# Kernel optimization log

Hardware: AMD Instinct MI355X
Metric: run time of the kernel (lower is better)

Reference implementation:

```python
import jax, jax.numpy as jnp
import numpy as np

GRID = 8        # proto_grid_size
THRESH = 0.95   # prototype selection threshold
EPS = 1e-4      # safe_norm eps
TEMP = 20.0     # cosine-similarity temperature
NEG_INF = -1e9

def safe_norm(x, axis):
    n = jnp.maximum(jnp.linalg.norm(x, axis=axis, keepdims=True), EPS)
    return x / n

def avg_pool(x, k):
    # [B, C, H, W] -> [B, C, H//k, W//k], non-overlapping average pooling
    B, C, H, W = x.shape
    return x.reshape(B, C, H // k, k, W // k, k).mean(axis=(3, 5))

def setup_inputs() -> dict:
    key = jax.random.key(0)
    k1, k2 = jax.random.split(key)
    qry = jax.random.normal(k1, (16, 512, 64, 64), dtype=jnp.float32)
    sup_x = jax.random.normal(k2, (16, 512, 64, 64), dtype=jnp.float32)
    sup_y = jnp.ones((16, 1, 64, 64), dtype=jnp.float32)
    return {"qry": qry, "sup_x": sup_x, "sup_y": sup_y}

def reference(qry, sup_x, sup_y):
    # mode='gridconv', thresh=0.95 (module defaults)
    B, C, H, W = sup_x.shape
    k = H // GRID  # avg-pool kernel size

    # normalize query features over channels (safe_norm with dim=1)
    qry_n = safe_norm(qry, axis=1)

    # grid prototypes: avg-pool support features, flatten to [B*G*G, C]
    n_sup = avg_pool(sup_x, k)                                   # [B, C, G, G]
    n_sup = n_sup.reshape(B, C, -1).transpose(0, 2, 1).reshape(-1, C)

    # pooled mask grid and thresholding
    sup_y_g = avg_pool(sup_y, k)                                 # [B, 1, G, G]
    proto_grid = jnp.where(sup_y_g < THRESH, 0.0, sup_y_g)
    valid = sup_y_g.reshape(-1) > THRESH                          # [P] bool

    # normalized prototypes (per-row; masking handles unselected cells)
    protos = safe_norm(n_sup, axis=1)                             # [P, C]

    # 1x1-conv similarity == channel contraction, scaled by temperature
    dists = jnp.einsum('bchw,pc->bphw', qry_n, protos) * TEMP     # [B, P, Hq, Wq]
    logits = jnp.where(valid[None, :, None, None], dists, NEG_INF)

    # softmax-weighted sum over prototypes (invalid protos get exactly 0 weight)
    p = jax.nn.softmax(logits, axis=1)
    vals = jnp.where(valid[None, :, None, None], dists, 0.0)
    pred = jnp.sum(p * vals, axis=1, keepdims=True)               # [B, 1, Hq, Wq]

    debug_assign = jnp.argmax(logits, axis=1).astype(jnp.float32)
    return pred, debug_assign, proto_grid
```

## Files before the change

### kernel.cpp

```cpp
#include <hip/hip_runtime.h>
#include <math.h>

#define B_      16
#define C_      512
#define HW_     4096
#define P_      1024
#define EPSN    1e-4f
#define TEMP_   20.0f
#define THRESH_ 0.95f
#define NEGINF_ -1e9f
#define TIE_THR 1e-3f

#define PRED_OFF   0
#define ASSIGN_OFF 65536
#define GRID_OFF   131072

typedef short short8 __attribute__((ext_vector_type(8)));
typedef float f32x16 __attribute__((ext_vector_type(16)));

__device__ inline unsigned short f2bf(float f) {
    unsigned u = __float_as_uint(f);
    unsigned r = u + 0x7fffu + ((u >> 16) & 1u);
    return (unsigned short)(r >> 16);
}
__device__ inline float bf2f(unsigned short h) {
    return __uint_as_float((unsigned)h << 16);
}

__global__ void pool_y_kernel(const float* __restrict__ sup_y,
                              float* __restrict__ out_grid,
                              float* __restrict__ validf) {
    int p = blockIdx.x * blockDim.x + threadIdx.x;
    if (p >= P_) return;
    int b = p >> 6, cell = p & 63, gy = cell >> 3, gx = cell & 7;
    const float* base = sup_y + b * HW_ + gy * 8 * 64 + gx * 8;
    float s = 0.f;
    #pragma unroll
    for (int r = 0; r < 8; ++r)
        #pragma unroll
        for (int c = 0; c < 8; ++c) s += base[r * 64 + c];
    float avg = s * (1.0f / 64.0f);
    out_grid[p] = (avg < THRESH_) ? 0.0f : avg;
    validf[p]   = (avg > THRESH_) ? 1.0f : 0.0f;
}

__global__ __launch_bounds__(256) void pool_x_kernel(const float* __restrict__ sup_x,
                                                     float* __restrict__ pooledT) {
    int blk = blockIdx.x * 4 + (threadIdx.x >> 6);
    int b = blk >> 9, c = blk & 511;
    int lane = threadIdx.x & 63;
    const float* base = sup_x + (size_t)(b * C_ + c) * HW_;
    float acc[8];
    #pragma unroll
    for (int g = 0; g < 8; ++g) acc[g] = 0.f;
    #pragma unroll
    for (int h = 0; h < 64; ++h) {
        float v = base[h * 64 + lane];
        acc[h >> 3] += v;
    }
    #pragma unroll
    for (int g = 0; g < 8; ++g) {
        acc[g] += __shfl_xor(acc[g], 1);
        acc[g] += __shfl_xor(acc[g], 2);
        acc[g] += __shfl_xor(acc[g], 4);
    }
    if ((lane & 7) == 0) {
        int gx = lane >> 3;
        #pragma unroll
        for (int gy = 0; gy < 8; ++gy) {
            int p = b * 64 + gy * 8 + gx;
            pooledT[c * P_ + p] = acc[gy] * (1.0f / 64.0f);
        }
    }
}

__global__ __launch_bounds__(512) void pack_b_kernel(const float* __restrict__ pooledT,
                                                     const float* __restrict__ validf,
                                                     short* __restrict__ Bph,
                                                     short* __restrict__ Bpl,
                                                     float* __restrict__ rnv) {
    __shared__ double ssred[8][64];
    int nl = threadIdx.x & 63;
    int w  = threadIdx.x >> 6;
    int n  = blockIdx.x * 64 + nl;
    double ss = 0.0;
    for (int c8i = 0; c8i < 8; ++c8i) {
        int c8 = w * 8 + c8i;
        unsigned short vh[8], vl[8];
        #pragma unroll
        for (int j = 0; j < 8; ++j) {
            float p = pooledT[(c8 * 8 + j) * P_ + n];
            ss += (double)p * (double)p;
            unsigned short h = f2bf(p);
            vh[j] = h;
            vl[j] = f2bf(p - bf2f(h));
        }
        uint4 uh, ul;
        uh.x = (unsigned)vh[0] | ((unsigned)vh[1] << 16);
        uh.y = (unsigned)vh[2] | ((unsigned)vh[3] << 16);
        uh.z = (unsigned)vh[4] | ((unsigned)vh[5] << 16);
        uh.w = (unsigned)vh[6] | ((unsigned)vh[7] << 16);
        ul.x = (unsigned)vl[0] | ((unsigned)vl[1] << 16);
        ul.y = (unsigned)vl[2] | ((unsigned)vl[3] << 16);
        ul.z = (unsigned)vl[4] | ((unsigned)vl[5] << 16);
        ul.w = (unsigned)vl[6] | ((unsigned)vl[7] << 16);
        int sk = c8 >> 1, kh = c8 & 1;
        *(uint4*)&Bph[sk * 16384 + n * 16 + kh * 8] = uh;
        *(uint4*)&Bpl[sk * 16384 + n * 16 + kh * 8] = ul;
    }
    ssred[w][nl] = ss;
    __syncthreads();
    if (threadIdx.x < 64) {
        double s = 0.0;
        #pragma unroll
        for (int q = 0; q < 8; ++q) s += ssred[q][threadIdx.x];
        int nn = blockIdx.x * 64 + threadIdx.x;
        float rn = 1.0f / fmaxf((float)sqrt(s), EPSN);
        rnv[nn] = (validf[nn] > 0.5f) ? rn : 0.0f;
    }
}

__global__ __launch_bounds__(512, 2) void gemm_fused_kernel(
        const float* __restrict__ qry,
        const short* __restrict__ Bph,
        const short* __restrict__ Bpl,
        const float* __restrict__ pooledT,
        const float* __restrict__ rnv,
        float* __restrict__ out) {
    __shared__ short Ah2[32 * 1024];
    __shared__ short Al2[32 * 1024];

    float* ss_tab  = (float*)Ah2;
    float* rq_s    = (float*)Ah2 + 512;
    float* stbuf   = (float*)Ah2 + 576;
    int*   rowinfo = (int*)((float*)Ah2 + 576 + 64 * 8 * 6);

    int m0 = blockIdx.x * 64;
    int b = m0 >> 12;
    int hw0 = m0 & 4095;
    int tid = threadIdx.x;
    int w = tid >> 6;
    int lane = tid & 63;
    int hl = lane & 31, half = lane >> 5;
    int nb = w * 128;

    const float* qb = qry + (size_t)b * (C_ * HW_) + hw0;
    const short* bh_base = Bph + ((nb + hl) * 16 + half * 8);
    const short* bl_base = Bpl + ((nb + hl) * 16 + half * 8);

    f32x16 zero16 = {0.f,0.f,0.f,0.f,0.f,0.f,0.f,0.f,0.f,0.f,0.f,0.f,0.f,0.f,0.f,0.f};
    f32x16 acc[2][4];
    #pragma unroll
    for (int mt = 0; mt < 2; ++mt)
        #pragma unroll
        for (int nt = 0; nt < 4; ++nt) acc[mt][nt] = zero16;

    short8 bhc[4], blc[4];
    #pragma unroll
    for (int nt = 0; nt < 4; ++nt) {
        bhc[nt] = *(const short8*)(bh_base + nt * 512);
        blc[nt] = *(const short8*)(bl_base + nt * 512);
    }

    float ss = 0.f;
    #pragma unroll
    for (int g = 0; g < 8; ++g) {
        int idx16 = g * 8 + w;
        const float* qp = qb + (size_t)(idx16 * 8) * HW_ + lane;
        float q[8];
        #pragma unroll
        for (int j = 0; j < 8; ++j) q[j] = qp[(size_t)j * HW_];
        uint4 UH, UL;
        unsigned uh[4], ul[4];
        #pragma unroll
        for (int jj = 0; jj < 4; ++jj) {
            float a0 = q[2 * jj], a1 = q[2 * jj + 1];
            unsigned short h0 = f2bf(a0), h1 = f2bf(a1);
            float r0 = a0 - bf2f(h0), r1 = a1 - bf2f(h1);
            unsigned short l0 = f2bf(r0), l1 = f2bf(r1);
            uh[jj] = (unsigned)h0 | ((unsigned)h1 << 16);
            ul[jj] = (unsigned)l0 | ((unsigned)l1 << 16);
            ss += a0 * a0 + a1 * a1;
        }
        UH.x = uh[0]; UH.y = uh[1]; UH.z = uh[2]; UH.w = uh[3];
        UL.x = ul[0]; UL.y = ul[1]; UL.z = ul[2]; UL.w = ul[3];
        int off = (idx16 * 64 + lane) * 8;
        *(uint4*)&Ah2[off] = UH;
        *(uint4*)&Al2[off] = UL;
    }
    __syncthreads();

    int abase = half * 512 + hl * 8;
    short8 ahc[2], alc[2];
    #pragma unroll
    for (int mt = 0; mt < 2; ++mt) {
        ahc[mt] = *(const short8*)&Ah2[abase + mt * 256];
        alc[mt] = *(const short8*)&Al2[abase + mt * 256];
    }

    for (int sk = 0; sk < 32; ++sk) {
        int nsk = sk + 1;
        short8 bhn[4], bln[4], ahn[2], aln[2];
        if (nsk < 32) {
            const short* bh_p = bh_base + nsk * 16384;
            const short* bl_p = bl_base + nsk * 16384;
            #pragma unroll
            for (int nt = 0; nt < 4; ++nt) {
                bhn[nt] = *(const short8*)(bh_p + nt * 512);
                bln[nt] = *(const short8*)(bl_p + nt * 512);
            }
            int ao = nsk * 1024 + abase;
            #pragma unroll
            for (int mt = 0; mt < 2; ++mt) {
                ahn[mt] = *(const short8*)&Ah2[ao + mt * 256];
                aln[mt] = *(const short8*)&Al2[ao + mt * 256];
            }
        }
        #pragma unroll
        for (int nt = 0; nt < 4; ++nt) {
            #pragma unroll
            for (int mt = 0; mt < 2; ++mt) {
                acc[mt][nt] = __builtin_amdgcn_mfma_f32_32x32x16_bf16(ahc[mt], bhc[nt], acc[mt][nt], 0, 0, 0);
                acc[mt][nt] = __builtin_amdgcn_mfma_f32_32x32x16_bf16(alc[mt], bhc[nt], acc[mt][nt], 0, 0, 0);
                acc[mt][nt] = __builtin_amdgcn_mfma_f32_32x32x16_bf16(ahc[mt], blc[nt], acc[mt][nt], 0, 0, 0);
            }
        }
        if (nsk < 32) {
            #pragma unroll
            for (int nt = 0; nt < 4; ++nt) { bhc[nt] = bhn[nt]; blc[nt] = bln[nt]; }
            #pragma unroll
            for (int mt = 0; mt < 2; ++mt) { ahc[mt] = ahn[mt]; alc[mt] = aln[mt]; }
        }
    }
    __syncthreads();

    ss_tab[w * 64 + lane] = ss;
    __syncthreads();
    if (tid < 64) {
        float s = 0.f;
        #pragma unroll
        for (int q = 0; q < 8; ++q) s += ss_tab[q * 64 + tid];
        rq_s[tid] = 1.0f / fmaxf(sqrtf(s), EPSN);
    }
    __syncthreads();

    float rn4[4];
    #pragma unroll
    for (int nt = 0; nt < 4; ++nt) rn4[nt] = rnv[nb + nt * 32 + hl];

    #pragma unroll
    for (int mt = 0; mt < 2; ++mt) {
        #pragma unroll
        for (int r = 0; r < 16; ++r) {
            int mrow = mt * 32 + (r & 3) + 8 * (r >> 2) + 4 * half;
            float scale = rq_s[mrow] * TEMP_;
            float d4[4], lg4[4];
            float v1 = -3e38f, v2 = -3e38f;
            int n1 = P_, n2 = P_;
            #pragma unroll
            for (int nt = 0; nt < 4; ++nt) {
                float dd = acc[mt][nt][r] * rn4[nt] * scale;
                float lg = (rn4[nt] > 0.f) ? dd : NEGINF_;
                d4[nt] = dd; lg4[nt] = lg;
                int n = nb + nt * 32 + hl;
                if (lg > v1 || (lg == v1 && n < n1)) {
                    v2 = v1; n2 = n1; v1 = lg; n1 = n;
                } else if (lg > v2 || (lg == v2 && n < n2)) {
                    v2 = lg; n2 = n;
                }
            }
            #pragma unroll
            for (int off = 1; off < 32; off <<= 1) {
                float ov1 = __shfl_xor(v1, off), ov2 = __shfl_xor(v2, off);
                int   on1 = __shfl_xor(n1, off), on2 = __shfl_xor(n2, off);
                if (ov1 > v1 || (ov1 == v1 && on1 < n1)) {
                    if (v1 > ov2 || (v1 == ov2 && n1 < on2)) { v2 = v1; n2 = n1; }
                    else                                     { v2 = ov2; n2 = on2; }
                    v1 = ov1; n1 = on1;
                } else {
                    if (ov1 > v2 || (ov1 == v2 && on1 < n2)) { v2 = ov1; n2 = on1; }
                }
            }
            float se = 0.f, sv = 0.f;
            #pragma unroll
            for (int nt = 0; nt < 4; ++nt) {
                float e = __expf(lg4[nt] - v1);
                se += e;
                sv += e * d4[nt];
            }
            #pragma unroll
            for (int off = 1; off < 32; off <<= 1) {
                se += __shfl_xor(se, off);
                sv += __shfl_xor(sv, off);
            }
            if (hl == 0) {
                float* s6 = stbuf + (mrow * 8 + w) * 6;
                s6[0] = v1; s6[1] = v2;
                s6[2] = __int_as_float(n1); s6[3] = __int_as_float(n2);
                s6[4] = se; s6[5] = sv;
            }
        }
    }
    __syncthreads();

    {
        int row = w * 8 + (lane >> 3), s = lane & 7;
        const float* s6 = stbuf + (row * 8 + s) * 6;
        float v1 = s6[0], v2 = s6[1];
        int n1 = __float_as_int(s6[2]), n2 = __float_as_int(s6[3]);
        float se = s6[4], sv = s6[5];
        #pragma unroll
        for (int off = 1; off < 8; off <<= 1) {
            float ov1 = __shfl_xor(v1, off), ov2 = __shfl_xor(v2, off);
            int   on1 = __shfl_xor(n1, off), on2 = __shfl_xor(n2, off);
            float ose = __shfl_xor(se, off), osv = __shfl_xor(sv, off);
            float myv1 = v1;
            float mv1, mv2; int mn1, mn2;
            if (ov1 > v1 || (ov1 == v1 && on1 < n1)) {
                mv1 = ov1; mn1 = on1;
                if (v1 > ov2 || (v1 == ov2 && n1 < on2)) { mv2 = v1; mn2 = n1; }
                else                                     { mv2 = ov2; mn2 = on2; }
            } else {
                mv1 = v1; mn1 = n1;
                if (ov1 > v2 || (ov1 == v2 && on1 < n2)) { mv2 = ov1; mn2 = on1; }
                else                                     { mv2 = v2; mn2 = n2; }
            }
            float fa = __expf(myv1 - mv1), fb = __expf(ov1 - mv1);
            se = se * fa + ose * fb;
            sv = sv * fa + osv * fb;
            v1 = mv1; n1 = mn1; v2 = mv2; n2 = mn2;
        }
        if (s == 0) {
            int gm = m0 + row;
            out[PRED_OFF + gm] = sv / se;
            bool flagged = (n2 < P_) && ((v1 - v2) < TIE_THR);
            if (!flagged) out[ASSIGN_OFF + gm] = (float)n1;
            rowinfo[row] = flagged ? (n1 | (n2 << 16)) : -1;
        }
    }
    __syncthreads();

    if (w == 0) {
        for (int row = 0; row < 64; ++row) {
            int info = rowinfo[row];
            if (info < 0) continue;
            int n1 = info & 0xffff, n2 = info >> 16;
            const float* qcol = qb + row;
            double d1 = 0.0, d2 = 0.0, s1 = 0.0, s2 = 0.0;
            for (int cc = lane; cc < C_; cc += 64) {
                double qv = (double)qcol[(size_t)cc * HW_];
                double p1 = (double)pooledT[cc * P_ + n1];
                double p2 = (double)pooledT[cc * P_ + n2];
                d1 += qv * p1; d2 += qv * p2;
                s1 += p1 * p1; s2 += p2 * p2;
            }
            #pragma unroll
            for (int off = 1; off < 64; off <<= 1) {
                d1 += __shfl_xor(d1, off); d2 += __shfl_xor(d2, off);
                s1 += __shfl_xor(s1, off); s2 += __shfl_xor(s2, off);
            }
            double f1 = d1 / fmax(sqrt(s1), (double)EPSN);
            double f2 = d2 / fmax(sqrt(s2), (double)EPSN);
            int best = (f2 > f1 || (f2 == f1 && n2 < n1)) ? n2 : n1;
            if (lane == 0) out[ASSIGN_OFF + m0 + row] = (float)best;
        }
    }
}

extern "C" void kernel_launch(void* const* d_in, const int* in_sizes, int n_in,
                              void* d_out, int out_size, void* d_ws, size_t ws_size,
                              hipStream_t stream) {
    const float* qry   = (const float*)d_in[0];
    const float* sup_x = (const float*)d_in[1];
    const float* sup_y = (const float*)d_in[2];
    float* out = (float*)d_out;
    float* ws  = (float*)d_ws;

    float* pooledT = ws;
    float* rnv     = pooledT + C_ * P_;
    float* validf  = rnv + P_;
    short* Bph     = (short*)(validf + P_);
    short* Bpl     = Bph + 32 * 1024 * 16;

    pool_y_kernel<<<4, 256, 0, stream>>>(sup_y, out + GRID_OFF, validf);
    pool_x_kernel<<<B_ * C_ / 4, 256, 0, stream>>>(sup_x, pooledT);
    pack_b_kernel<<<16, 512, 0, stream>>>(pooledT, validf, Bph, Bpl, rnv);
    gemm_fused_kernel<<<B_ * HW_ / 64, 512, 0, stream>>>(qry, Bph, Bpl, pooledT, rnv, out);
}
```

Measured before the change: 642.3 us.

## Vectorize pooling and query loads, double-buffer MFMA operands with setprio

```diff
diff --git a/kernel.cpp b/kernel.cpp
--- a/kernel.cpp
+++ b/kernel.cpp
@@ -49,28 +49,28 @@
     int blk = blockIdx.x * 4 + (threadIdx.x >> 6);
     int b = blk >> 9, c = blk & 511;
     int lane = threadIdx.x & 63;
+    int cq = lane & 15, rq = lane >> 4;
     const float* base = sup_x + (size_t)(b * C_ + c) * HW_;
     float acc[8];
     #pragma unroll
     for (int g = 0; g < 8; ++g) acc[g] = 0.f;
     #pragma unroll
-    for (int h = 0; h < 64; ++h) {
-        float v = base[h * 64 + lane];
-        acc[h >> 3] += v;
+    for (int i = 0; i < 16; ++i) {
+        int row = 4 * i + rq;
+        float4 v = *(const float4*)(base + row * 64 + cq * 4);
+        acc[i >> 1] += (v.x + v.y) + (v.z + v.w);
     }
     #pragma unroll
     for (int g = 0; g < 8; ++g) {
         acc[g] += __shfl_xor(acc[g], 1);
-        acc[g] += __shfl_xor(acc[g], 2);
-        acc[g] += __shfl_xor(acc[g], 4);
-    }
-    if ((lane & 7) == 0) {
-        int gx = lane >> 3;
-        #pragma unroll
-        for (int gy = 0; gy < 8; ++gy) {
-            int p = b * 64 + gy * 8 + gx;
-            pooledT[c * P_ + p] = acc[gy] * (1.0f / 64.0f);
-        }
+        acc[g] += __shfl_xor(acc[g], 16);
+        acc[g] += __shfl_xor(acc[g], 32);
+    }
+    if (rq == 0 && (cq & 1) == 0) {
+        int gx = cq >> 1;
+        #pragma unroll
+        for (int gy = 0; gy < 8; ++gy)
+            pooledT[c * P_ + b * 64 + gy * 8 + gx] = acc[gy] * (1.0f / 64.0f);
     }
 }
 
@@ -129,11 +129,11 @@
         float* __restrict__ out) {
     __shared__ short Ah2[32 * 1024];
     __shared__ short Al2[32 * 1024];
-
-    float* ss_tab  = (float*)Ah2;
-    float* rq_s    = (float*)Ah2 + 512;
-    float* stbuf   = (float*)Ah2 + 576;
-    int*   rowinfo = (int*)((float*)Ah2 + 576 + 64 * 8 * 6);
+    __shared__ float ss_part[512 * 4];
+    __shared__ float rqs_lds[64];
+
+    float* stbuf   = (float*)Ah2;
+    int*   rowinfo = (int*)((float*)Ah2 + 64 * 8 * 6);
 
     int m0 = blockIdx.x * 64;
     int b = m0 >> 12;
@@ -155,92 +155,122 @@
         #pragma unroll
         for (int nt = 0; nt < 4; ++nt) acc[mt][nt] = zero16;
 
-    short8 bhc[4], blc[4];
+    short8 bh0[4], bl0[4], bh1[4], bl1[4];
+    short8 ah0[2], al0[2], ah1[2], al1[2];
     #pragma unroll
     for (int nt = 0; nt < 4; ++nt) {
-        bhc[nt] = *(const short8*)(bh_base + nt * 512);
-        blc[nt] = *(const short8*)(bl_base + nt * 512);
-    }
-
-    float ss = 0.f;
-    #pragma unroll
-    for (int g = 0; g < 8; ++g) {
-        int idx16 = g * 8 + w;
-        const float* qp = qb + (size_t)(idx16 * 8) * HW_ + lane;
-        float q[8];
-        #pragma unroll
-        for (int j = 0; j < 8; ++j) q[j] = qp[(size_t)j * HW_];
-        uint4 UH, UL;
-        unsigned uh[4], ul[4];
-        #pragma unroll
-        for (int jj = 0; jj < 4; ++jj) {
-            float a0 = q[2 * jj], a1 = q[2 * jj + 1];
-            unsigned short h0 = f2bf(a0), h1 = f2bf(a1);
-            float r0 = a0 - bf2f(h0), r1 = a1 - bf2f(h1);
-            unsigned short l0 = f2bf(r0), l1 = f2bf(r1);
-            uh[jj] = (unsigned)h0 | ((unsigned)h1 << 16);
-            ul[jj] = (unsigned)l0 | ((unsigned)l1 << 16);
-            ss += a0 * a0 + a1 * a1;
-        }
-        UH.x = uh[0]; UH.y = uh[1]; UH.z = uh[2]; UH.w = uh[3];
-        UL.x = ul[0]; UL.y = ul[1]; UL.z = ul[2]; UL.w = ul[3];
-        int off = (idx16 * 64 + lane) * 8;
-        *(uint4*)&Ah2[off] = UH;
-        *(uint4*)&Al2[off] = UL;
+        bh0[nt] = *(const short8*)(bh_base + nt * 512);
+        bl0[nt] = *(const short8*)(bl_base + nt * 512);
+    }
+
+    {
+        int pg = tid & 15;
+        int c8a = tid >> 4;
+        float ss4[4] = {0.f, 0.f, 0.f, 0.f};
+        #pragma unroll
+        for (int un = 0; un < 2; ++un) {
+            int c8 = c8a + un * 32;
+            const float* src = qb + (size_t)(c8 * 8) * HW_ + pg * 4;
+            float4 q[8];
+            #pragma unroll
+            for (int j = 0; j < 8; ++j)
+                q[j] = *(const float4*)(src + (size_t)j * HW_);
+            #pragma unroll
+            for (int pp = 0; pp < 4; ++pp) {
+                unsigned uh[4], ul[4];
+                #pragma unroll
+                for (int jj = 0; jj < 4; ++jj) {
+                    float a0 = ((const float*)&q[2 * jj])[pp];
+                    float a1 = ((const float*)&q[2 * jj + 1])[pp];
+                    unsigned short h0 = f2bf(a0), h1 = f2bf(a1);
+                    float r0 = a0 - bf2f(h0), r1 = a1 - bf2f(h1);
+                    unsigned short l0 = f2bf(r0), l1 = f2bf(r1);
+                    uh[jj] = (unsigned)h0 | ((unsigned)h1 << 16);
+                    ul[jj] = (unsigned)l0 | ((unsigned)l1 << 16);
+                    ss4[pp] += a0 * a0 + a1 * a1;
+                }
+                uint4 UH, UL;
+                UH.x = uh[0]; UH.y = uh[1]; UH.z = uh[2]; UH.w = uh[3];
+                UL.x = ul[0]; UL.y = ul[1]; UL.z = ul[2]; UL.w = ul[3];
+                int off = (c8 * 64 + pg * 4 + pp) * 8;
+                *(uint4*)&Ah2[off] = UH;
+                *(uint4*)&Al2[off] = UL;
+            }
+        }
+        *(float4*)&ss_part[tid * 4] = *(float4*)ss4;
     }
     __syncthreads();
 
+    if (tid < 64) {
+        int pg = tid >> 2, pp = tid & 3;
+        float s = 0.f;
+        #pragma unroll
+        for (int k = 0; k < 32; ++k) s += ss_part[(pg + 16 * k) * 4 + pp];
+        rqs_lds[tid] = 1.0f / fmaxf(sqrtf(s), EPSN);
+    }
+
     int abase = half * 512 + hl * 8;
-    short8 ahc[2], alc[2];
     #pragma unroll
     for (int mt = 0; mt < 2; ++mt) {
-        ahc[mt] = *(const short8*)&Ah2[abase + mt * 256];
-        alc[mt] = *(const short8*)&Al2[abase + mt * 256];
-    }
-
-    for (int sk = 0; sk < 32; ++sk) {
-        int nsk = sk + 1;
-        short8 bhn[4], bln[4], ahn[2], aln[2];
-        if (nsk < 32) {
-            const short* bh_p = bh_base + nsk * 16384;
-            const short* bl_p = bl_base + nsk * 16384;
+        ah0[mt] = *(const short8*)&Ah2[abase + mt * 256];
+        al0[mt] = *(const short8*)&Al2[abase + mt * 256];
+    }
+
+    for (int skp = 0; skp < 16; ++skp) {
+        int sk1 = skp * 2 + 1;
+        int sk2 = (skp < 15) ? (skp * 2 + 2) : 31;
+        {
+            const short* bh_p = bh_base + sk1 * 16384;
+            const short* bl_p = bl_base + sk1 * 16384;
             #pragma unroll
             for (int nt = 0; nt < 4; ++nt) {
-                bhn[nt] = *(const short8*)(bh_p + nt * 512);
-                bln[nt] = *(const short8*)(bl_p + nt * 512);
-            }
-            int ao = nsk * 1024 + abase;
+                bh1[nt] = *(const short8*)(bh_p + nt * 512);
+                bl1[nt] = *(const short8*)(bl_p + nt * 512);
+            }
+            int ao = sk1 * 1024 + abase;
             #pragma unroll
             for (int mt = 0; mt < 2; ++mt) {
-                ahn[mt] = *(const short8*)&Ah2[ao + mt * 256];
-                aln[mt] = *(const short8*)&Al2[ao + mt * 256];
-            }
-        }
+                ah1[mt] = *(const short8*)&Ah2[ao + mt * 256];
+                al1[mt] = *(const short8*)&Al2[ao + mt * 256];
+            }
+        }
+        __builtin_amdgcn_s_setprio(1);
         #pragma unroll
         for (int nt = 0; nt < 4; ++nt) {
             #pragma unroll
             for (int mt = 0; mt < 2; ++mt) {
-                acc[mt][nt] = __builtin_amdgcn_mfma_f32_32x32x16_bf16(ahc[mt], bhc[nt], acc[mt][nt], 0, 0, 0);
-                acc[mt][nt] = __builtin_amdgcn_mfma_f32_32x32x16_bf16(alc[mt], bhc[nt], acc[mt][nt], 0, 0, 0);
-                acc[mt][nt] = __builtin_amdgcn_mfma_f32_32x32x16_bf16(ahc[mt], blc[nt], acc[mt][nt], 0, 0, 0);
-            }
-        }
-        if (nsk < 32) {
-            #pragma unroll
-            for (int nt = 0; nt < 4; ++nt) { bhc[nt] = bhn[nt]; blc[nt] = bln[nt]; }
-            #pragma unroll
-            for (int mt = 0; mt < 2; ++mt) { ahc[mt] = ahn[mt]; alc[mt] = aln[mt]; }
-        }
-    }
-    __syncthreads();
-
-    ss_tab[w * 64 + lane] = ss;
-    __syncthreads();
-    if (tid < 64) {
-        float s = 0.f;
-        #pragma unroll
-        for (int q = 0; q < 8; ++q) s += ss_tab[q * 64 + tid];
-        rq_s[tid] = 1.0f / fmaxf(sqrtf(s), EPSN);
+                acc[mt][nt] = __builtin_amdgcn_mfma_f32_32x32x16_bf16(ah0[mt], bh0[nt], acc[mt][nt], 0, 0, 0);
+                acc[mt][nt] = __builtin_amdgcn_mfma_f32_32x32x16_bf16(al0[mt], bh0[nt], acc[mt][nt], 0, 0, 0);
+                acc[mt][nt] = __builtin_amdgcn_mfma_f32_32x32x16_bf16(ah0[mt], bl0[nt], acc[mt][nt], 0, 0, 0);
+            }
+        }
+        __builtin_amdgcn_s_setprio(0);
+        {
+            const short* bh_p = bh_base + sk2 * 16384;
+            const short* bl_p = bl_base + sk2 * 16384;
+            #pragma unroll
+            for (int nt = 0; nt < 4; ++nt) {
+                bh0[nt] = *(const short8*)(bh_p + nt * 512);
+                bl0[nt] = *(const short8*)(bl_p + nt * 512);
+            }
+            int ao = sk2 * 1024 + abase;
+            #pragma unroll
+            for (int mt = 0; mt < 2; ++mt) {
+                ah0[mt] = *(const short8*)&Ah2[ao + mt * 256];
+                al0[mt] = *(const short8*)&Al2[ao + mt * 256];
+            }
+        }
+        __builtin_amdgcn_s_setprio(1);
+        #pragma unroll
+        for (int nt = 0; nt < 4; ++nt) {
+            #pragma unroll
+            for (int mt = 0; mt < 2; ++mt) {
+                acc[mt][nt] = __builtin_amdgcn_mfma_f32_32x32x16_bf16(ah1[mt], bh1[nt], acc[mt][nt], 0, 0, 0);
+                acc[mt][nt] = __builtin_amdgcn_mfma_f32_32x32x16_bf16(al1[mt], bh1[nt], acc[mt][nt], 0, 0, 0);
+                acc[mt][nt] = __builtin_amdgcn_mfma_f32_32x32x16_bf16(ah1[mt], bl1[nt], acc[mt][nt], 0, 0, 0);
+            }
+        }
+        __builtin_amdgcn_s_setprio(0);
     }
     __syncthreads();
 
@@ -253,7 +283,7 @@
         #pragma unroll
         for (int r = 0; r < 16; ++r) {
             int mrow = mt * 32 + (r & 3) + 8 * (r >> 2) + 4 * half;
-            float scale = rq_s[mrow] * TEMP_;
+            float scale = rqs_lds[mrow] * TEMP_;
             float d4[4], lg4[4];
             float v1 = -3e38f, v2 = -3e38f;
             int n1 = P_, n2 = P_;
```

Result: no change. 646.6 us (+0.7%).

## Stream query A-tile through smaller LDS buffer in four phases with float4 loads

Applied to the files above, without the earlier changes.

```diff
diff --git a/kernel.cpp b/kernel.cpp
--- a/kernel.cpp
+++ b/kernel.cpp
@@ -49,28 +49,28 @@
     int blk = blockIdx.x * 4 + (threadIdx.x >> 6);
     int b = blk >> 9, c = blk & 511;
     int lane = threadIdx.x & 63;
+    int cq = lane & 15, rq = lane >> 4;
     const float* base = sup_x + (size_t)(b * C_ + c) * HW_;
     float acc[8];
     #pragma unroll
     for (int g = 0; g < 8; ++g) acc[g] = 0.f;
     #pragma unroll
-    for (int h = 0; h < 64; ++h) {
-        float v = base[h * 64 + lane];
-        acc[h >> 3] += v;
+    for (int i = 0; i < 16; ++i) {
+        int row = 4 * i + rq;
+        float4 v = *(const float4*)(base + row * 64 + cq * 4);
+        acc[i >> 1] += (v.x + v.y) + (v.z + v.w);
     }
     #pragma unroll
     for (int g = 0; g < 8; ++g) {
         acc[g] += __shfl_xor(acc[g], 1);
-        acc[g] += __shfl_xor(acc[g], 2);
-        acc[g] += __shfl_xor(acc[g], 4);
-    }
-    if ((lane & 7) == 0) {
-        int gx = lane >> 3;
-        #pragma unroll
-        for (int gy = 0; gy < 8; ++gy) {
-            int p = b * 64 + gy * 8 + gx;
-            pooledT[c * P_ + p] = acc[gy] * (1.0f / 64.0f);
-        }
+        acc[g] += __shfl_xor(acc[g], 16);
+        acc[g] += __shfl_xor(acc[g], 32);
+    }
+    if (rq == 0 && (cq & 1) == 0) {
+        int gx = cq >> 1;
+        #pragma unroll
+        for (int gy = 0; gy < 8; ++gy)
+            pooledT[c * P_ + b * 64 + gy * 8 + gx] = acc[gy] * (1.0f / 64.0f);
     }
 }
 
@@ -127,13 +127,11 @@
         const float* __restrict__ pooledT,
         const float* __restrict__ rnv,
         float* __restrict__ out) {
-    __shared__ short Ah2[32 * 1024];
-    __shared__ short Al2[32 * 1024];
-
-    float* ss_tab  = (float*)Ah2;
-    float* rq_s    = (float*)Ah2 + 512;
-    float* stbuf   = (float*)Ah2 + 576;
-    int*   rowinfo = (int*)((float*)Ah2 + 576 + 64 * 8 * 6);
+    __shared__ short A_lds[16 * 64 * 8 * 2];
+    __shared__ float rqs_lds[64];
+    __shared__ int rowinfo[64];
+    float* ss_part = (float*)A_lds;
+    float* stbuf   = (float*)A_lds + 2048;
 
     int m0 = blockIdx.x * 64;
     int b = m0 >> 12;
@@ -162,85 +160,102 @@
         blc[nt] = *(const short8*)(bl_base + nt * 512);
     }
 
-    float ss = 0.f;
-    #pragma unroll
-    for (int g = 0; g < 8; ++g) {
-        int idx16 = g * 8 + w;
-        const float* qp = qb + (size_t)(idx16 * 8) * HW_ + lane;
-        float q[8];
-        #pragma unroll
-        for (int j = 0; j < 8; ++j) q[j] = qp[(size_t)j * HW_];
-        uint4 UH, UL;
-        unsigned uh[4], ul[4];
-        #pragma unroll
-        for (int jj = 0; jj < 4; ++jj) {
-            float a0 = q[2 * jj], a1 = q[2 * jj + 1];
-            unsigned short h0 = f2bf(a0), h1 = f2bf(a1);
-            float r0 = a0 - bf2f(h0), r1 = a1 - bf2f(h1);
-            unsigned short l0 = f2bf(r0), l1 = f2bf(r1);
-            uh[jj] = (unsigned)h0 | ((unsigned)h1 << 16);
-            ul[jj] = (unsigned)l0 | ((unsigned)l1 << 16);
-            ss += a0 * a0 + a1 * a1;
-        }
-        UH.x = uh[0]; UH.y = uh[1]; UH.z = uh[2]; UH.w = uh[3];
-        UL.x = ul[0]; UL.y = ul[1]; UL.z = ul[2]; UL.w = ul[3];
-        int off = (idx16 * 64 + lane) * 8;
-        *(uint4*)&Ah2[off] = UH;
-        *(uint4*)&Al2[off] = UL;
-    }
-    __syncthreads();
-
-    int abase = half * 512 + hl * 8;
+    int pg = tid & 15;
+    int u  = tid >> 4;
+    float ss4[4] = {0.f, 0.f, 0.f, 0.f};
     short8 ahc[2], alc[2];
-    #pragma unroll
-    for (int mt = 0; mt < 2; ++mt) {
-        ahc[mt] = *(const short8*)&Ah2[abase + mt * 256];
-        alc[mt] = *(const short8*)&Al2[abase + mt * 256];
-    }
-
-    for (int sk = 0; sk < 32; ++sk) {
-        int nsk = sk + 1;
-        short8 bhn[4], bln[4], ahn[2], aln[2];
-        if (nsk < 32) {
-            const short* bh_p = bh_base + nsk * 16384;
-            const short* bl_p = bl_base + nsk * 16384;
+
+    for (int T = 0; T < 4; ++T) {
+        if (T) __syncthreads();
+        if ((u >> 4) == (T & 1)) {
+            int c8 = u + (T >> 1) * 32;
+            int c8l = c8 & 15;
+            const float* src = qb + (size_t)(c8 * 8) * HW_ + pg * 4;
+            float4 q[8];
+            #pragma unroll
+            for (int j = 0; j < 8; ++j)
+                q[j] = *(const float4*)(src + (size_t)j * HW_);
+            #pragma unroll
+            for (int pp = 0; pp < 4; ++pp) {
+                unsigned uh[4], ul[4];
+                #pragma unroll
+                for (int jj = 0; jj < 4; ++jj) {
+                    float a0 = ((const float*)&q[2 * jj])[pp];
+                    float a1 = ((const float*)&q[2 * jj + 1])[pp];
+                    unsigned short h0 = f2bf(a0), h1 = f2bf(a1);
+                    float r0 = a0 - bf2f(h0), r1 = a1 - bf2f(h1);
+                    unsigned short l0 = f2bf(r0), l1 = f2bf(r1);
+                    uh[jj] = (unsigned)h0 | ((unsigned)h1 << 16);
+                    ul[jj] = (unsigned)l0 | ((unsigned)l1 << 16);
+                    ss4[pp] += a0 * a0 + a1 * a1;
+                }
+                uint4 UH, UL;
+                UH.x = uh[0]; UH.y = uh[1]; UH.z = uh[2]; UH.w = uh[3];
+                UL.x = ul[0]; UL.y = ul[1]; UL.z = ul[2]; UL.w = ul[3];
+                int off = (c8l * 64 + pg * 4 + pp) * 8;
+                *(uint4*)&A_lds[off] = UH;
+                *(uint4*)&A_lds[8192 + off] = UL;
+            }
+        }
+        __syncthreads();
+
+        int ab0 = (half * 64 + hl) * 8;
+        #pragma unroll
+        for (int mt = 0; mt < 2; ++mt) {
+            ahc[mt] = *(const short8*)&A_lds[ab0 + mt * 256];
+            alc[mt] = *(const short8*)&A_lds[8192 + ab0 + mt * 256];
+        }
+
+        for (int s = 0; s < 8; ++s) {
+            int sk = T * 8 + s;
+            int nsk = sk + 1;
+            short8 bhn[4], bln[4], ahn[2], aln[2];
+            if (nsk < 32) {
+                const short* bh_p = bh_base + nsk * 16384;
+                const short* bl_p = bl_base + nsk * 16384;
+                #pragma unroll
+                for (int nt = 0; nt < 4; ++nt) {
+                    bhn[nt] = *(const short8*)(bh_p + nt * 512);
+                    bln[nt] = *(const short8*)(bl_p + nt * 512);
+                }
+            }
+            if (s < 7) {
+                int abn = (((s + 1) * 2 + half) * 64 + hl) * 8;
+                #pragma unroll
+                for (int mt = 0; mt < 2; ++mt) {
+                    ahn[mt] = *(const short8*)&A_lds[abn + mt * 256];
+                    aln[mt] = *(const short8*)&A_lds[8192 + abn + mt * 256];
+                }
+            }
             #pragma unroll
             for (int nt = 0; nt < 4; ++nt) {
-                bhn[nt] = *(const short8*)(bh_p + nt * 512);
-                bln[nt] = *(const short8*)(bl_p + nt * 512);
-            }
-            int ao = nsk * 1024 + abase;
-            #pragma unroll
-            for (int mt = 0; mt < 2; ++mt) {
-                ahn[mt] = *(const short8*)&Ah2[ao + mt * 256];
-                aln[mt] = *(const short8*)&Al2[ao + mt * 256];
-            }
-        }
-        #pragma unroll
-        for (int nt = 0; nt < 4; ++nt) {
-            #pragma unroll
-            for (int mt = 0; mt < 2; ++mt) {
-                acc[mt][nt] = __builtin_amdgcn_mfma_f32_32x32x16_bf16(ahc[mt], bhc[nt], acc[mt][nt], 0, 0, 0);
-                acc[mt][nt] = __builtin_amdgcn_mfma_f32_32x32x16_bf16(alc[mt], bhc[nt], acc[mt][nt], 0, 0, 0);
-                acc[mt][nt] = __builtin_amdgcn_mfma_f32_32x32x16_bf16(ahc[mt], blc[nt], acc[mt][nt], 0, 0, 0);
-            }
-        }
-        if (nsk < 32) {
-            #pragma unroll
-            for (int nt = 0; nt < 4; ++nt) { bhc[nt] = bhn[nt]; blc[nt] = bln[nt]; }
-            #pragma unroll
-            for (int mt = 0; mt < 2; ++mt) { ahc[mt] = ahn[mt]; alc[mt] = aln[mt]; }
-        }
-    }
-    __syncthreads();
-
-    ss_tab[w * 64 + lane] = ss;
+                #pragma unroll
+                for (int mt = 0; mt < 2; ++mt) {
+                    acc[mt][nt] = __builtin_amdgcn_mfma_f32_32x32x16_bf16(ahc[mt], bhc[nt], acc[mt][nt], 0, 0, 0);
+                    acc[mt][nt] = __builtin_amdgcn_mfma_f32_32x32x16_bf16(alc[mt], bhc[nt], acc[mt][nt], 0, 0, 0);
+                    acc[mt][nt] = __builtin_amdgcn_mfma_f32_32x32x16_bf16(ahc[mt], blc[nt], acc[mt][nt], 0, 0, 0);
+                }
+            }
+            if (nsk < 32) {
+                #pragma unroll
+                for (int nt = 0; nt < 4; ++nt) { bhc[nt] = bhn[nt]; blc[nt] = bln[nt]; }
+            }
+            if (s < 7) {
+                #pragma unroll
+                for (int mt = 0; mt < 2; ++mt) { ahc[mt] = ahn[mt]; alc[mt] = aln[mt]; }
+            }
+        }
+    }
+    __syncthreads();
+
+    *(float4*)&ss_part[tid * 4] = *(const float4*)ss4;
     __syncthreads();
     if (tid < 64) {
+        int pg2 = tid >> 2, pp = tid & 3;
         float s = 0.f;
         #pragma unroll
-        for (int q = 0; q < 8; ++q) s += ss_tab[q * 64 + tid];
-        rq_s[tid] = 1.0f / fmaxf(sqrtf(s), EPSN);
+        for (int k = 0; k < 32; ++k) s += ss_part[(pg2 + 16 * k) * 4 + pp];
+        rqs_lds[tid] = 1.0f / fmaxf(sqrtf(s), EPSN);
     }
     __syncthreads();
 
@@ -253,7 +268,7 @@
         #pragma unroll
         for (int r = 0; r < 16; ++r) {
             int mrow = mt * 32 + (r & 3) + 8 * (r >> 2) + 4 * half;
-            float scale = rq_s[mrow] * TEMP_;
+            float scale = rqs_lds[mrow] * TEMP_;
             float d4[4], lg4[4];
             float v1 = -3e38f, v2 = -3e38f;
             int n1 = P_, n2 = P_;
```

Measured after the change: 1.016 ms. 58.3% more time.
